# Kernel tuning notes

Measured on AMD Instinct MI355X. Metric: run time of the kernel, lower is better.

The kernel has to match this reference:

```python
import jax, jax.numpy as jnp
import numpy as np

D_MODEL, D_STATE, D_INNER, DT_RANK, K = 64, 16, 128, 4, 4
EPS = 1e-6  # RMSNorm eps


def setup_inputs() -> dict:
    key = jax.random.key(0)
    ks = jax.random.split(key, 12)
    B, L = 8, 4096
    s = 0.02
    x = jax.random.normal(ks[0], (B, L, D_MODEL), dtype=jnp.float32)
    w_norm = jnp.ones((D_MODEL,), jnp.float32)
    W_in = jax.random.normal(ks[1], (2 * D_INNER, D_MODEL), jnp.float32) * s
    b_in = jnp.zeros((2 * D_INNER,), jnp.float32)
    W_conv = jax.random.normal(ks[2], (D_INNER, D_INNER, K), jnp.float32) * s
    b_conv = jnp.zeros((D_INNER,), jnp.float32)
    W_xp = jax.random.normal(ks[3], (DT_RANK + 2 * D_STATE, D_INNER), jnp.float32) * s
    b_xp = jnp.zeros((DT_RANK + 2 * D_STATE,), jnp.float32)
    W_dt = jax.random.normal(ks[4], (D_INNER, DT_RANK), jnp.float32) * s
    b_dt = jnp.zeros((D_INNER,), jnp.float32)
    W_out = jax.random.normal(ks[5], (D_MODEL, D_INNER), jnp.float32) * s
    b_out = jnp.zeros((D_MODEL,), jnp.float32)
    A_log = jnp.log(jnp.tile(jnp.arange(1, D_STATE + 1, dtype=jnp.float32), (D_INNER, 1)))
    D_param = jnp.ones((D_INNER,), jnp.float32)
    return dict(x=x, w_norm=w_norm, W_in=W_in, b_in=b_in, W_conv=W_conv, b_conv=b_conv,
                W_xp=W_xp, b_xp=b_xp, W_dt=W_dt, b_dt=b_dt, W_out=W_out, b_out=b_out,
                A_log=A_log, D_param=D_param)


def _mamba_block(xn, W_in, b_in, W_conv, b_conv, W_xp, b_xp, W_dt, b_dt, W_out, b_out, A_log, D_param):
    B, L, _ = xn.shape
    xz = xn @ W_in.T + b_in                      # (B,L,2*d_inner)
    u, z = jnp.split(xz, 2, axis=-1)
    z = jax.nn.silu(z)
    # conv1d: NCH, causal-style pad (K-1) both sides then truncate to L
    uc = jax.lax.conv_general_dilated(
        u.transpose(0, 2, 1), W_conv, window_strides=(1,), padding=[(K - 1, K - 1)],
        dimension_numbers=("NCH", "OIH", "NCH"))[:, :, :L] + b_conv[None, :, None]
    u = jax.nn.silu(uc.transpose(0, 2, 1))       # (B,L,d_inner)
    xp = u @ W_xp.T + b_xp
    dt, Bm, Cm = jnp.split(xp, [DT_RANK, DT_RANK + D_STATE], axis=-1)
    delta = jax.nn.softplus(dt @ W_dt.T + b_dt)  # (B,L,d_inner)
    A = -jnp.exp(A_log)                          # (d_inner, n)
    A_bar = jnp.exp(jnp.einsum('bld,dn->bldn', delta, A))
    B_bar_x = jnp.einsum('bld,bln,bld->bldn', delta, Bm, u)

    def step(h, inp):
        a, bx, c = inp                           # (B,d,n),(B,d,n),(B,n)
        h = a * h + bx
        y = jnp.einsum('bdn,bn->bd', h, c)
        return h, y

    h0 = jnp.zeros((B, D_INNER, D_STATE), xn.dtype)
    xs = (A_bar.transpose(1, 0, 2, 3), B_bar_x.transpose(1, 0, 2, 3), Cm.transpose(1, 0, 2))
    _, ys = jax.lax.scan(step, h0, xs)           # (L,B,d_inner)
    y = ys.transpose(1, 0, 2) + D_param * u
    y = y * z
    return y @ W_out.T + b_out


def reference(x, w_norm, W_in, b_in, W_conv, b_conv, W_xp, b_xp, W_dt, b_dt, W_out, b_out, A_log, D_param):
    xn = x * jax.lax.rsqrt(jnp.mean(x * x, axis=-1, keepdims=True) + EPS) * w_norm
    return x + _mamba_block(xn, W_in, b_in, W_conv, b_conv, W_xp, b_xp, W_dt, b_dt, W_out, b_out, A_log, D_param)
```

## Files before the change

kernel.cpp:

```cpp
#include <hip/hip_runtime.h>
#include <math.h>

#define D_MODEL 64
#define D_STATE 16
#define D_INNER 128
#define DT_RANK 4
#define BB 8
#define LL 4096
#define NTOK (BB*LL)
#define EPSV 1e-6f
#define NCHUNK 64
#define LC (LL/NCHUNK)
#define PAD 136

typedef __attribute__((ext_vector_type(8))) short bf16x8;
typedef __attribute__((ext_vector_type(4))) float f32x4;

__device__ __forceinline__ float sig_(float v) { return 1.f / (1.f + __expf(-v)); }
__device__ __forceinline__ float softplus_(float v) {
    return (v > 20.f) ? v : __logf(1.f + __expf(v));
}
__device__ __forceinline__ unsigned short f2bf(float x) {
    unsigned int u = __float_as_uint(x);
    u += 0x7fff + ((u >> 16) & 1);
    return (unsigned short)(u >> 16);
}
__device__ __forceinline__ float bf2f(unsigned short u) {
    return __uint_as_float(((unsigned int)u) << 16);
}
__device__ __forceinline__ unsigned int pack2bf(float a, float b) {
    return (unsigned int)f2bf(a) | ((unsigned int)f2bf(b) << 16);
}

__global__ __launch_bounds__(256) void pack_all(
    const float* __restrict__ W_in, const float* __restrict__ w_norm,
    const float* __restrict__ W_conv, const float* __restrict__ W_xp,
    const float* __restrict__ W_out,
    unsigned short* __restrict__ Win_bf, unsigned short* __restrict__ Bp,
    unsigned short* __restrict__ Wxp_bf, unsigned short* __restrict__ Wout_bf)
{
    int i = blockIdx.x * 256 + threadIdx.x;
    if (i < 16384) {
        Win_bf[i] = f2bf(W_in[i] * w_norm[i & 63]);
    } else if (i < 81920) {
        int j = i - 16384;
        int kk = j >> 14, o = (j >> 7) & 127, c = j & 127;
        Bp[j] = f2bf(W_conv[o * 512 + c * 4 + kk]);
    } else if (i < 88064) {
        int j = i - 81920;
        Wxp_bf[j] = ((j >> 7) < 36) ? f2bf(W_xp[j]) : (unsigned short)0;
    } else if (i < 96256) {
        int j = i - 88064;
        Wout_bf[j] = f2bf(W_out[j]);
    }
}

__global__ __launch_bounds__(256) void k1_fused(
    const float* __restrict__ x, const unsigned short* __restrict__ Win_bf,
    const float* __restrict__ b_in,
    unsigned short* __restrict__ u_bf, unsigned short* __restrict__ z_bf)
{
    __shared__ unsigned short axs[64 * 72];
    int tid = threadIdx.x;
    int tb = blockIdx.x * 64;
    {
        int t = tid >> 2, qt = tid & 3;
        float4 v[4];
        float ss = 0.f;
        #pragma unroll
        for (int j = 0; j < 4; ++j) {
            v[j] = *(const float4*)&x[(tb + t) * 64 + qt * 16 + j * 4];
            ss += v[j].x*v[j].x + v[j].y*v[j].y + v[j].z*v[j].z + v[j].w*v[j].w;
        }
        ss += __shfl_xor(ss, 1, 64);
        ss += __shfl_xor(ss, 2, 64);
        float r = rsqrtf(ss * (1.f / 64.f) + EPSV);
        unsigned short tmp[16];
        #pragma unroll
        for (int j = 0; j < 4; ++j) {
            tmp[4*j+0] = f2bf(v[j].x * r); tmp[4*j+1] = f2bf(v[j].y * r);
            tmp[4*j+2] = f2bf(v[j].z * r); tmp[4*j+3] = f2bf(v[j].w * r);
        }
        *(bf16x8*)&axs[t * 72 + qt * 16]     = *(bf16x8*)&tmp[0];
        *(bf16x8*)&axs[t * 72 + qt * 16 + 8] = *(bf16x8*)&tmp[8];
    }
    __syncthreads();
    int wave = tid >> 6, lane = tid & 63;
    int quad = lane >> 4, l16 = lane & 15;
    f32x4 acc[16];
    #pragma unroll
    for (int nt = 0; nt < 16; ++nt) acc[nt] = (f32x4){0.f, 0.f, 0.f, 0.f};
    bf16x8 a0 = *(const bf16x8*)&axs[(wave * 16 + l16) * 72 + quad * 8];
    bf16x8 a1 = *(const bf16x8*)&axs[(wave * 16 + l16) * 72 + 32 + quad * 8];
    #pragma unroll
    for (int nt = 0; nt < 16; ++nt) {
        bf16x8 b0 = *(const bf16x8*)&Win_bf[(nt * 16 + l16) * 64 + quad * 8];
        bf16x8 b1 = *(const bf16x8*)&Win_bf[(nt * 16 + l16) * 64 + 32 + quad * 8];
        acc[nt] = __builtin_amdgcn_mfma_f32_16x16x32_bf16(a0, b0, acc[nt], 0, 0, 0);
        acc[nt] = __builtin_amdgcn_mfma_f32_16x16x32_bf16(a1, b1, acc[nt], 0, 0, 0);
    }
    #pragma unroll
    for (int nt = 0; nt < 16; ++nt) {
        int o = nt * 16 + l16;
        float bo = b_in[o];
        #pragma unroll
        for (int r = 0; r < 4; ++r) {
            int t = tb + wave * 16 + quad * 4 + r;
            float v = acc[nt][r] + bo;
            if (o < 128) u_bf[t * 128 + o] = f2bf(v);
            else         z_bf[t * 128 + (o - 128)] = f2bf(v * sig_(v));
        }
    }
}

__global__ __launch_bounds__(256) void k2k3a_fused(
    const unsigned short* __restrict__ u_bf, const unsigned short* __restrict__ Bp,
    const float* __restrict__ b_conv,
    const unsigned short* __restrict__ Wxp_bf, const float* __restrict__ b_xp,
    const float* __restrict__ W_dt, const float* __restrict__ b_dt,
    const float* __restrict__ A_log,
    unsigned short* __restrict__ u_cbf, unsigned short* __restrict__ delta_bf,
    float* __restrict__ Bm, float* __restrict__ Cm,
    float* __restrict__ P, float* __restrict__ Q)
{
    __shared__ unsigned short uls[64 * PAD];
    __shared__ unsigned short dls[64 * PAD];
    __shared__ float bls[64 * 16];
    __shared__ float dts[64][4];
    __shared__ float Wd[512];
    __shared__ float bds[128];
    int tid = threadIdx.x;
    if (tid < 128) *(float4*)&Wd[tid * 4] = *(const float4*)&W_dt[tid * 4];
    else if (tid < 160) *(float4*)&bds[(tid - 128) * 4] = *(const float4*)&b_dt[(tid - 128) * 4];
    int wave = tid >> 6, lane = tid & 63;
    int quad = lane >> 4, l16 = lane & 15;
    int tb = blockIdx.x * 64;
    int bbase = tb & ~4095;
    int t0 = tb + wave * 16;
    f32x4 acc[8];
    #pragma unroll
    for (int og = 0; og < 8; ++og) acc[og] = (f32x4){0.f, 0.f, 0.f, 0.f};
    int row_base = t0 + l16 - 3;
    #pragma unroll
    for (int kk = 0; kk < 4; ++kk) {
        int row = row_base + kk;
        #pragma unroll
        for (int cs = 0; cs < 4; ++cs) {
            int kbase = cs * 32 + quad * 8;
            bf16x8 a = {0,0,0,0,0,0,0,0};
            if (row >= bbase)
                a = *(const bf16x8*)&u_bf[row * 128 + kbase];
            #pragma unroll
            for (int og = 0; og < 8; ++og) {
                bf16x8 b = *(const bf16x8*)&Bp[kk * 16384 + (og * 16 + l16) * 128 + kbase];
                acc[og] = __builtin_amdgcn_mfma_f32_16x16x32_bf16(a, b, acc[og], 0, 0, 0);
            }
        }
    }
    #pragma unroll
    for (int og = 0; og < 8; ++og) {
        int o = og * 16 + l16;
        float bc = b_conv[o];
        #pragma unroll
        for (int r = 0; r < 4; ++r) {
            int tloc = wave * 16 + quad * 4 + r;
            float v = acc[og][r] + bc;
            unsigned short ub = f2bf(v * sig_(v));
            u_cbf[(tb + tloc) * 128 + o] = ub;
            uls[tloc * PAD + o] = ub;
        }
    }
    __syncthreads();
    f32x4 xacc[3];
    #pragma unroll
    for (int nt = 0; nt < 3; ++nt) xacc[nt] = (f32x4){0.f, 0.f, 0.f, 0.f};
    #pragma unroll
    for (int cs = 0; cs < 4; ++cs) {
        int kbase = cs * 32 + quad * 8;
        bf16x8 a = *(const bf16x8*)&uls[(wave * 16 + l16) * PAD + kbase];
        #pragma unroll
        for (int nt = 0; nt < 3; ++nt) {
            bf16x8 b = *(const bf16x8*)&Wxp_bf[(nt * 16 + l16) * 128 + kbase];
            xacc[nt] = __builtin_amdgcn_mfma_f32_16x16x32_bf16(a, b, xacc[nt], 0, 0, 0);
        }
    }
    #pragma unroll
    for (int nt = 0; nt < 3; ++nt) {
        int j = nt * 16 + l16;
        float bx = (j < 36) ? b_xp[j] : 0.f;
        #pragma unroll
        for (int r = 0; r < 4; ++r) {
            int tloc = wave * 16 + quad * 4 + r;
            int t = tb + tloc;
            float val = xacc[nt][r] + bx;
            if (j < 4) {
                dts[tloc][j] = val;
            } else if (j < 20) {
                Bm[t * 16 + (j - 4)] = val;
                bls[tloc * 16 + (j - 4)] = val;
            } else if (j < 36) {
                Cm[t * 16 + (j - 20)] = val;
            }
        }
    }
    __syncthreads();
    {
        int tokloc = tid >> 2, dgrp = tid & 3;
        float dt0 = dts[tokloc][0], dt1 = dts[tokloc][1],
              dt2 = dts[tokloc][2], dt3 = dts[tokloc][3];
        int g = tb + tokloc;
        #pragma unroll
        for (int d4 = 0; d4 < 8; ++d4) {
            int d = dgrp * 32 + d4 * 4;
            float4 w0 = *(const float4*)&Wd[(d + 0) * 4];
            float4 w1 = *(const float4*)&Wd[(d + 1) * 4];
            float4 w2 = *(const float4*)&Wd[(d + 2) * 4];
            float4 w3 = *(const float4*)&Wd[(d + 3) * 4];
            float4 bdv = *(const float4*)&bds[d];
            float4 r;
            r.x = softplus_(bdv.x + dt0*w0.x + dt1*w0.y + dt2*w0.z + dt3*w0.w);
            r.y = softplus_(bdv.y + dt0*w1.x + dt1*w1.y + dt2*w1.z + dt3*w1.w);
            r.z = softplus_(bdv.z + dt0*w2.x + dt1*w2.y + dt2*w2.z + dt3*w2.w);
            r.w = softplus_(bdv.w + dt0*w3.x + dt1*w3.y + dt2*w3.z + dt3*w3.w);
            uint2 pk; pk.x = pack2bf(r.x, r.y); pk.y = pack2bf(r.z, r.w);
            *(uint2*)&delta_bf[g * 128 + d] = pk;
            *(uint2*)&dls[tokloc * PAD + d] = pk;
        }
    }
    __syncthreads();
    {
        int d = tid >> 1;
        int nb = (tid & 1) * 8;
        float4 Av0 = *(const float4*)&A_log[d * 16 + nb];
        float4 Av1 = *(const float4*)&A_log[d * 16 + nb + 4];
        float A0 = -__expf(Av0.x), A1 = -__expf(Av0.y),
              A2 = -__expf(Av0.z), A3 = -__expf(Av0.w);
        float A4 = -__expf(Av1.x), A5 = -__expf(Av1.y),
              A6 = -__expf(Av1.z), A7 = -__expf(Av1.w);
        float P0=1.f,P1=1.f,P2=1.f,P3=1.f,P4=1.f,P5=1.f,P6=1.f,P7=1.f;
        float Q0=0.f,Q1=0.f,Q2=0.f,Q3=0.f,Q4=0.f,Q5=0.f,Q6=0.f,Q7=0.f;
        for (int t = 0; t < LC; ++t) {
            float dl = bf2f(dls[t * PAD + d]);
            float uu = bf2f(uls[t * PAD + d]);
            float4 bm0 = *(const float4*)&bls[t * 16 + nb];
            float4 bm1 = *(const float4*)&bls[t * 16 + nb + 4];
            float du = dl * uu;
            float a0 = __expf(dl * A0), a1 = __expf(dl * A1),
                  a2 = __expf(dl * A2), a3 = __expf(dl * A3);
            float a4 = __expf(dl * A4), a5 = __expf(dl * A5),
                  a6 = __expf(dl * A6), a7 = __expf(dl * A7);
            P0 *= a0; P1 *= a1; P2 *= a2; P3 *= a3;
            P4 *= a4; P5 *= a5; P6 *= a6; P7 *= a7;
            Q0 = a0 * Q0 + du * bm0.x; Q1 = a1 * Q1 + du * bm0.y;
            Q2 = a2 * Q2 + du * bm0.z; Q3 = a3 * Q3 + du * bm0.w;
            Q4 = a4 * Q4 + du * bm1.x; Q5 = a5 * Q5 + du * bm1.y;
            Q6 = a6 * Q6 + du * bm1.z; Q7 = a7 * Q7 + du * bm1.w;
        }
        int idx = blockIdx.x * 2048 + d * 16 + nb;
        *(float4*)&P[idx]     = (float4){P0, P1, P2, P3};
        *(float4*)&P[idx + 4] = (float4){P4, P5, P6, P7};
        *(float4*)&Q[idx]     = (float4){Q0, Q1, Q2, Q3};
        *(float4*)&Q[idx + 4] = (float4){Q4, Q5, Q6, Q7};
    }
}

__global__ __launch_bounds__(256) void k4b_carry(
    const float* __restrict__ P, const float* __restrict__ Q, float* __restrict__ Hinit)
{
    int tid = blockIdx.x * 256 + threadIdx.x;
    int b = tid >> 11, dn = tid & 2047;
    float carry = 0.f;
    for (int c0 = 0; c0 < NCHUNK; c0 += 8) {
        float p[8], q[8];
        #pragma unroll
        for (int j = 0; j < 8; ++j) {
            int idx = (b * NCHUNK + c0 + j) * 2048 + dn;
            p[j] = P[idx]; q[j] = Q[idx];
        }
        #pragma unroll
        for (int j = 0; j < 8; ++j) {
            int idx = (b * NCHUNK + c0 + j) * 2048 + dn;
            Hinit[idx] = carry;
            carry = p[j] * carry + q[j];
        }
    }
}

__global__ __launch_bounds__(256) void k4c5_fused(
    const unsigned short* __restrict__ delta_bf, const unsigned short* __restrict__ u_cbf,
    const float* __restrict__ Bm, const float* __restrict__ Cm,
    const unsigned short* __restrict__ z_bf, const float* __restrict__ A_log,
    const float* __restrict__ D_param, const float* __restrict__ Hinit,
    const unsigned short* __restrict__ Wout_bf, const float* __restrict__ b_out,
    const float* __restrict__ x, float* __restrict__ out)
{
    __shared__ unsigned short dls[LC * 128];
    __shared__ unsigned short uls[LC * 128];
    __shared__ float bls[LC * 16];
    __shared__ float cls[LC * 16];
    __shared__ unsigned short yzls[LC * PAD];
    int bid = blockIdx.x;
    int tid = threadIdx.x, lane = tid & 63;
    int g0 = bid * 64;
    for (int i = tid; i < LC * 16; i += 256) {
        int row = i >> 4, q = i & 15;
        *(float4*)&dls[row * 128 + q * 8] =
            *(const float4*)&delta_bf[(g0 + row) * 128 + q * 8];
        *(float4*)&uls[row * 128 + q * 8] =
            *(const float4*)&u_cbf[(g0 + row) * 128 + q * 8];
        *(float4*)&yzls[row * PAD + q * 8] =
            *(const float4*)&z_bf[(g0 + row) * 128 + q * 8];
    }
    for (int i = tid; i < LC * 4; i += 256) {
        int row = i >> 2, q = i & 3;
        *(float4*)&bls[row * 16 + q * 4] = *(const float4*)&Bm[(g0 + row) * 16 + q * 4];
        *(float4*)&cls[row * 16 + q * 4] = *(const float4*)&Cm[(g0 + row) * 16 + q * 4];
    }
    int d = tid >> 1;
    int nb = (tid & 1) * 8;
    float4 Av0 = *(const float4*)&A_log[d * 16 + nb];
    float4 Av1 = *(const float4*)&A_log[d * 16 + nb + 4];
    float A0 = -__expf(Av0.x), A1 = -__expf(Av0.y), A2 = -__expf(Av0.z), A3 = -__expf(Av0.w);
    float A4 = -__expf(Av1.x), A5 = -__expf(Av1.y), A6 = -__expf(Av1.z), A7 = -__expf(Av1.w);
    int hbase = bid * 2048 + d * 16 + nb;
    float4 h0 = *(const float4*)&Hinit[hbase];
    float4 h1 = *(const float4*)&Hinit[hbase + 4];
    float Dp = D_param[d];
    __syncthreads();
    for (int t = 0; t < LC; ++t) {
        float dl = bf2f(dls[t * 128 + d]);
        float uu = bf2f(uls[t * 128 + d]);
        float4 bm0 = *(const float4*)&bls[t * 16 + nb];
        float4 bm1 = *(const float4*)&bls[t * 16 + nb + 4];
        float4 cm0 = *(const float4*)&cls[t * 16 + nb];
        float4 cm1 = *(const float4*)&cls[t * 16 + nb + 4];
        float du = dl * uu;
        float a0 = __expf(dl * A0), a1 = __expf(dl * A1),
              a2 = __expf(dl * A2), a3 = __expf(dl * A3);
        float a4 = __expf(dl * A4), a5 = __expf(dl * A5),
              a6 = __expf(dl * A6), a7 = __expf(dl * A7);
        h0.x = a0 * h0.x + du * bm0.x; h0.y = a1 * h0.y + du * bm0.y;
        h0.z = a2 * h0.z + du * bm0.z; h0.w = a3 * h0.w + du * bm0.w;
        h1.x = a4 * h1.x + du * bm1.x; h1.y = a5 * h1.y + du * bm1.y;
        h1.z = a6 * h1.z + du * bm1.z; h1.w = a7 * h1.w + du * bm1.w;
        float yv = h0.x * cm0.x + h0.y * cm0.y + h0.z * cm0.z + h0.w * cm0.w
                 + h1.x * cm1.x + h1.y * cm1.y + h1.z * cm1.z + h1.w * cm1.w;
        yv += __shfl_xor(yv, 1, 64);
        if ((tid & 1) == 0) {
            float y = yv + Dp * uu;
            y *= bf2f(yzls[t * PAD + d]);
            yzls[t * PAD + d] = f2bf(y);
        }
    }
    __syncthreads();
    int wave = tid >> 6;
    int quad = lane >> 4, l16 = lane & 15;
    f32x4 oacc[4];
    #pragma unroll
    for (int nt = 0; nt < 4; ++nt) oacc[nt] = (f32x4){0.f, 0.f, 0.f, 0.f};
    #pragma unroll
    for (int cs = 0; cs < 4; ++cs) {
        int kbase = cs * 32 + quad * 8;
        bf16x8 a = *(const bf16x8*)&yzls[(wave * 16 + l16) * PAD + kbase];
        #pragma unroll
        for (int nt = 0; nt < 4; ++nt) {
            bf16x8 bb = *(const bf16x8*)&Wout_bf[(nt * 16 + l16) * 128 + kbase];
            oacc[nt] = __builtin_amdgcn_mfma_f32_16x16x32_bf16(a, bb, oacc[nt], 0, 0, 0);
        }
    }
    #pragma unroll
    for (int nt = 0; nt < 4; ++nt) {
        int m = nt * 16 + l16;
        float bo = b_out[m];
        #pragma unroll
        for (int r = 0; r < 4; ++r) {
            int t = g0 + wave * 16 + quad * 4 + r;
            out[t * 64 + m] = oacc[nt][r] + bo + x[t * 64 + m];
        }
    }
}

extern "C" void kernel_launch(void* const* d_in, const int* in_sizes, int n_in,
                              void* d_out, int out_size, void* d_ws, size_t ws_size,
                              hipStream_t stream)
{
    const float* x       = (const float*)d_in[0];
    const float* w_norm  = (const float*)d_in[1];
    const float* W_in    = (const float*)d_in[2];
    const float* b_in    = (const float*)d_in[3];
    const float* W_conv  = (const float*)d_in[4];
    const float* b_conv  = (const float*)d_in[5];
    const float* W_xp    = (const float*)d_in[6];
    const float* b_xp    = (const float*)d_in[7];
    const float* W_dt    = (const float*)d_in[8];
    const float* b_dt    = (const float*)d_in[9];
    const float* W_out   = (const float*)d_in[10];
    const float* b_out   = (const float*)d_in[11];
    const float* A_log   = (const float*)d_in[12];
    const float* D_param = (const float*)d_in[13];
    float* ws = (float*)d_ws;

    unsigned short* u_bf = (unsigned short*)ws;
    unsigned short* z_bf = (unsigned short*)(ws + 2097152);
    unsigned short* u_cbf= (unsigned short*)(ws + 4194304);
    unsigned short* delta_bf = (unsigned short*)(ws + 6291456);
    float* Bm     = ws + 10485760;
    float* Cm     = ws + 11010048;
    float* P      = ws + 11534336;
    float* Q      = ws + 12582912;
    float* Hinit  = ws + 13631488;
    unsigned short* Bp      = (unsigned short*)(ws + 14680064);
    unsigned short* Wxp_bf  = (unsigned short*)(ws + 14712832);
    unsigned short* Wout_bf = (unsigned short*)(ws + 14715904);
    unsigned short* Win_bf  = (unsigned short*)(ws + 14720000);
    float* out    = (float*)d_out;

    pack_all<<<376, 256, 0, stream>>>(W_in, w_norm, W_conv, W_xp, W_out,
                                      Win_bf, Bp, Wxp_bf, Wout_bf);
    k1_fused<<<512, 256, 0, stream>>>(x, Win_bf, b_in, u_bf, z_bf);
    k2k3a_fused<<<512, 256, 0, stream>>>(u_bf, Bp, b_conv, Wxp_bf, b_xp,
                                         W_dt, b_dt, A_log,
                                         u_cbf, delta_bf, Bm, Cm, P, Q);
    k4b_carry<<<64, 256, 0, stream>>>(P, Q, Hinit);
    k4c5_fused<<<512, 256, 0, stream>>>(delta_bf, u_cbf, Bm, Cm, z_bf, A_log,
                                        D_param, Hinit, Wout_bf, b_out, x, out);
}
```

Before: 184.0 us.

## Fuse RMSNorm+in_proj into conv/x_proj kernel with halo recompute

New measurement: 175.3 us. 4.7% less time.

```diff
diff --git a/kernel.cpp b/kernel.cpp
--- a/kernel.cpp
+++ b/kernel.cpp
@@ -55,80 +55,28 @@
     }
 }
 
-__global__ __launch_bounds__(256) void k1_fused(
+__global__ __launch_bounds__(256) void k123a_fused(
     const float* __restrict__ x, const unsigned short* __restrict__ Win_bf,
     const float* __restrict__ b_in,
-    unsigned short* __restrict__ u_bf, unsigned short* __restrict__ z_bf)
-{
-    __shared__ unsigned short axs[64 * 72];
-    int tid = threadIdx.x;
-    int tb = blockIdx.x * 64;
-    {
-        int t = tid >> 2, qt = tid & 3;
-        float4 v[4];
-        float ss = 0.f;
-        #pragma unroll
-        for (int j = 0; j < 4; ++j) {
-            v[j] = *(const float4*)&x[(tb + t) * 64 + qt * 16 + j * 4];
-            ss += v[j].x*v[j].x + v[j].y*v[j].y + v[j].z*v[j].z + v[j].w*v[j].w;
-        }
-        ss += __shfl_xor(ss, 1, 64);
-        ss += __shfl_xor(ss, 2, 64);
-        float r = rsqrtf(ss * (1.f / 64.f) + EPSV);
-        unsigned short tmp[16];
-        #pragma unroll
-        for (int j = 0; j < 4; ++j) {
-            tmp[4*j+0] = f2bf(v[j].x * r); tmp[4*j+1] = f2bf(v[j].y * r);
-            tmp[4*j+2] = f2bf(v[j].z * r); tmp[4*j+3] = f2bf(v[j].w * r);
-        }
-        *(bf16x8*)&axs[t * 72 + qt * 16]     = *(bf16x8*)&tmp[0];
-        *(bf16x8*)&axs[t * 72 + qt * 16 + 8] = *(bf16x8*)&tmp[8];
-    }
-    __syncthreads();
-    int wave = tid >> 6, lane = tid & 63;
-    int quad = lane >> 4, l16 = lane & 15;
-    f32x4 acc[16];
-    #pragma unroll
-    for (int nt = 0; nt < 16; ++nt) acc[nt] = (f32x4){0.f, 0.f, 0.f, 0.f};
-    bf16x8 a0 = *(const bf16x8*)&axs[(wave * 16 + l16) * 72 + quad * 8];
-    bf16x8 a1 = *(const bf16x8*)&axs[(wave * 16 + l16) * 72 + 32 + quad * 8];
-    #pragma unroll
-    for (int nt = 0; nt < 16; ++nt) {
-        bf16x8 b0 = *(const bf16x8*)&Win_bf[(nt * 16 + l16) * 64 + quad * 8];
-        bf16x8 b1 = *(const bf16x8*)&Win_bf[(nt * 16 + l16) * 64 + 32 + quad * 8];
-        acc[nt] = __builtin_amdgcn_mfma_f32_16x16x32_bf16(a0, b0, acc[nt], 0, 0, 0);
-        acc[nt] = __builtin_amdgcn_mfma_f32_16x16x32_bf16(a1, b1, acc[nt], 0, 0, 0);
-    }
-    #pragma unroll
-    for (int nt = 0; nt < 16; ++nt) {
-        int o = nt * 16 + l16;
-        float bo = b_in[o];
-        #pragma unroll
-        for (int r = 0; r < 4; ++r) {
-            int t = tb + wave * 16 + quad * 4 + r;
-            float v = acc[nt][r] + bo;
-            if (o < 128) u_bf[t * 128 + o] = f2bf(v);
-            else         z_bf[t * 128 + (o - 128)] = f2bf(v * sig_(v));
-        }
-    }
-}
-
-__global__ __launch_bounds__(256) void k2k3a_fused(
-    const unsigned short* __restrict__ u_bf, const unsigned short* __restrict__ Bp,
-    const float* __restrict__ b_conv,
+    const unsigned short* __restrict__ Bp, const float* __restrict__ b_conv,
     const unsigned short* __restrict__ Wxp_bf, const float* __restrict__ b_xp,
     const float* __restrict__ W_dt, const float* __restrict__ b_dt,
     const float* __restrict__ A_log,
-    unsigned short* __restrict__ u_cbf, unsigned short* __restrict__ delta_bf,
+    unsigned short* __restrict__ z_bf, unsigned short* __restrict__ u_cbf,
+    unsigned short* __restrict__ delta_bf,
     float* __restrict__ Bm, float* __restrict__ Cm,
     float* __restrict__ P, float* __restrict__ Q)
 {
-    __shared__ unsigned short uls[64 * PAD];
-    __shared__ unsigned short dls[64 * PAD];
-    __shared__ float bls[64 * 16];
-    __shared__ float dts[64][4];
-    __shared__ float Wd[512];
-    __shared__ float bds[128];
+    __shared__ unsigned char smem[54832];
+    unsigned short* axs  = (unsigned short*)smem;
+    unsigned short* upre = (unsigned short*)(smem + 11520);
+    unsigned short* dls  = upre;
+    unsigned short* uls  = (unsigned short*)(smem + 29744);
+    float* bls = (float*)(smem + 47152);
+    float (*dts)[4] = (float(*)[4])(smem + 51248);
+    float* Wd  = (float*)(smem + 52272);
+    float* bds = (float*)(smem + 54320);
+
     int tid = threadIdx.x;
     if (tid < 128) *(float4*)&Wd[tid * 4] = *(const float4*)&W_dt[tid * 4];
     else if (tid < 160) *(float4*)&bds[(tid - 128) * 4] = *(const float4*)&b_dt[(tid - 128) * 4];
@@ -136,70 +84,138 @@
     int quad = lane >> 4, l16 = lane & 15;
     int tb = blockIdx.x * 64;
     int bbase = tb & ~4095;
-    int t0 = tb + wave * 16;
-    f32x4 acc[8];
+
     #pragma unroll
-    for (int og = 0; og < 8; ++og) acc[og] = (f32x4){0.f, 0.f, 0.f, 0.f};
-    int row_base = t0 + l16 - 3;
+    for (int p = 0; p < 2; ++p) {
+        int lrow = p * 64 + (tid >> 2);
+        if (lrow < 67) {
+            int qt = tid & 3;
+            int g = tb - 3 + lrow;
+            float4 v[4];
+            float ss = 0.f;
+            if (g >= bbase) {
+                #pragma unroll
+                for (int j = 0; j < 4; ++j) {
+                    v[j] = *(const float4*)&x[g * 64 + qt * 16 + j * 4];
+                    ss += v[j].x*v[j].x + v[j].y*v[j].y + v[j].z*v[j].z + v[j].w*v[j].w;
+                }
+            } else {
+                #pragma unroll
+                for (int j = 0; j < 4; ++j) v[j] = (float4){0.f, 0.f, 0.f, 0.f};
+            }
+            ss += __shfl_xor(ss, 1, 64);
+            ss += __shfl_xor(ss, 2, 64);
+            float r = rsqrtf(ss * (1.f / 64.f) + EPSV);
+            unsigned short tmp[16];
+            #pragma unroll
+            for (int j = 0; j < 4; ++j) {
+                tmp[4*j+0] = f2bf(v[j].x * r); tmp[4*j+1] = f2bf(v[j].y * r);
+                tmp[4*j+2] = f2bf(v[j].z * r); tmp[4*j+3] = f2bf(v[j].w * r);
+            }
+            *(bf16x8*)&axs[lrow * 72 + qt * 16]     = *(bf16x8*)&tmp[0];
+            *(bf16x8*)&axs[lrow * 72 + qt * 16 + 8] = *(bf16x8*)&tmp[8];
+        }
+    }
+    __syncthreads();
     #pragma unroll
-    for (int kk = 0; kk < 4; ++kk) {
-        int row = row_base + kk;
+    for (int mt = 0; mt < 5; ++mt) {
+        bf16x8 a0 = *(const bf16x8*)&axs[(mt * 16 + l16) * 72 + quad * 8];
+        bf16x8 a1 = *(const bf16x8*)&axs[(mt * 16 + l16) * 72 + 32 + quad * 8];
+        f32x4 acc[4];
+        #pragma unroll
+        for (int nk = 0; nk < 4; ++nk) acc[nk] = (f32x4){0.f, 0.f, 0.f, 0.f};
+        #pragma unroll
+        for (int nk = 0; nk < 4; ++nk) {
+            int nt = wave * 4 + nk;
+            bf16x8 b0 = *(const bf16x8*)&Win_bf[(nt * 16 + l16) * 64 + quad * 8];
+            bf16x8 b1 = *(const bf16x8*)&Win_bf[(nt * 16 + l16) * 64 + 32 + quad * 8];
+            acc[nk] = __builtin_amdgcn_mfma_f32_16x16x32_bf16(a0, b0, acc[nk], 0, 0, 0);
+            acc[nk] = __builtin_amdgcn_mfma_f32_16x16x32_bf16(a1, b1, acc[nk], 0, 0, 0);
+        }
+        #pragma unroll
+        for (int nk = 0; nk < 4; ++nk) {
+            int o = (wave * 4 + nk) * 16 + l16;
+            float bo = b_in[o];
+            #pragma unroll
+            for (int r = 0; r < 4; ++r) {
+                int lrow = mt * 16 + quad * 4 + r;
+                if (lrow < 67) {
+                    float v = acc[nk][r] + bo;
+                    if (o < 128) {
+                        upre[lrow * PAD + o] = f2bf(v);
+                    } else if (lrow >= 3) {
+                        float zv = v * sig_(v);
+                        z_bf[(tb + lrow - 3) * 128 + (o - 128)] = f2bf(zv);
+                    }
+                }
+            }
+        }
+    }
+    __syncthreads();
+    {
+        f32x4 acc[8];
+        #pragma unroll
+        for (int og = 0; og < 8; ++og) acc[og] = (f32x4){0.f, 0.f, 0.f, 0.f};
+        #pragma unroll
+        for (int kk = 0; kk < 4; ++kk) {
+            int lr = wave * 16 + l16 + kk;
+            #pragma unroll
+            for (int cs = 0; cs < 4; ++cs) {
+                int kbase = cs * 32 + quad * 8;
+                bf16x8 a = *(const bf16x8*)&upre[lr * PAD + kbase];
+                #pragma unroll
+                for (int og = 0; og < 8; ++og) {
+                    bf16x8 b = *(const bf16x8*)&Bp[kk * 16384 + (og * 16 + l16) * 128 + kbase];
+                    acc[og] = __builtin_amdgcn_mfma_f32_16x16x32_bf16(a, b, acc[og], 0, 0, 0);
+                }
+            }
+        }
+        #pragma unroll
+        for (int og = 0; og < 8; ++og) {
+            int o = og * 16 + l16;
+            float bc = b_conv[o];
+            #pragma unroll
+            for (int r = 0; r < 4; ++r) {
+                int tloc = wave * 16 + quad * 4 + r;
+                float v = acc[og][r] + bc;
+                unsigned short ub = f2bf(v * sig_(v));
+                u_cbf[(tb + tloc) * 128 + o] = ub;
+                uls[tloc * PAD + o] = ub;
+            }
+        }
+    }
+    __syncthreads();
+    {
+        f32x4 xacc[3];
+        #pragma unroll
+        for (int nt = 0; nt < 3; ++nt) xacc[nt] = (f32x4){0.f, 0.f, 0.f, 0.f};
         #pragma unroll
         for (int cs = 0; cs < 4; ++cs) {
             int kbase = cs * 32 + quad * 8;
-            bf16x8 a = {0,0,0,0,0,0,0,0};
-            if (row >= bbase)
-                a = *(const bf16x8*)&u_bf[row * 128 + kbase];
-            #pragma unroll
-            for (int og = 0; og < 8; ++og) {
-                bf16x8 b = *(const bf16x8*)&Bp[kk * 16384 + (og * 16 + l16) * 128 + kbase];
-                acc[og] = __builtin_amdgcn_mfma_f32_16x16x32_bf16(a, b, acc[og], 0, 0, 0);
-            }
-        }
-    }
-    #pragma unroll
-    for (int og = 0; og < 8; ++og) {
-        int o = og * 16 + l16;
-        float bc = b_conv[o];
-        #pragma unroll
-        for (int r = 0; r < 4; ++r) {
-            int tloc = wave * 16 + quad * 4 + r;
-            float v = acc[og][r] + bc;
-            unsigned short ub = f2bf(v * sig_(v));
-            u_cbf[(tb + tloc) * 128 + o] = ub;
-            uls[tloc * PAD + o] = ub;
-        }
-    }
-    __syncthreads();
-    f32x4 xacc[3];
-    #pragma unroll
-    for (int nt = 0; nt < 3; ++nt) xacc[nt] = (f32x4){0.f, 0.f, 0.f, 0.f};
-    #pragma unroll
-    for (int cs = 0; cs < 4; ++cs) {
-        int kbase = cs * 32 + quad * 8;
-        bf16x8 a = *(const bf16x8*)&uls[(wave * 16 + l16) * PAD + kbase];
+            bf16x8 a = *(const bf16x8*)&uls[(wave * 16 + l16) * PAD + kbase];
+            #pragma unroll
+            for (int nt = 0; nt < 3; ++nt) {
+                bf16x8 b = *(const bf16x8*)&Wxp_bf[(nt * 16 + l16) * 128 + kbase];
+                xacc[nt] = __builtin_amdgcn_mfma_f32_16x16x32_bf16(a, b, xacc[nt], 0, 0, 0);
+            }
+        }
         #pragma unroll
         for (int nt = 0; nt < 3; ++nt) {
-            bf16x8 b = *(const bf16x8*)&Wxp_bf[(nt * 16 + l16) * 128 + kbase];
-            xacc[nt] = __builtin_amdgcn_mfma_f32_16x16x32_bf16(a, b, xacc[nt], 0, 0, 0);
-        }
-    }
-    #pragma unroll
-    for (int nt = 0; nt < 3; ++nt) {
-        int j = nt * 16 + l16;
-        float bx = (j < 36) ? b_xp[j] : 0.f;
-        #pragma unroll
-        for (int r = 0; r < 4; ++r) {
-            int tloc = wave * 16 + quad * 4 + r;
-            int t = tb + tloc;
-            float val = xacc[nt][r] + bx;
-            if (j < 4) {
-                dts[tloc][j] = val;
-            } else if (j < 20) {
-                Bm[t * 16 + (j - 4)] = val;
-                bls[tloc * 16 + (j - 4)] = val;
-            } else if (j < 36) {
-                Cm[t * 16 + (j - 20)] = val;
+            int j = nt * 16 + l16;
+            float bx = (j < 36) ? b_xp[j] : 0.f;
+            #pragma unroll
+            for (int r = 0; r < 4; ++r) {
+                int tloc = wave * 16 + quad * 4 + r;
+                int t = tb + tloc;
+                float val = xacc[nt][r] + bx;
+                if (j < 4) {
+                    dts[tloc][j] = val;
+                } else if (j < 20) {
+                    Bm[t * 16 + (j - 4)] = val;
+                    bls[tloc * 16 + (j - 4)] = val;
+                } else if (j < 36) {
+                    Cm[t * 16 + (j - 20)] = val;
+                }
             }
         }
     }
@@ -400,27 +416,25 @@
     const float* D_param = (const float*)d_in[13];
     float* ws = (float*)d_ws;
 
-    unsigned short* u_bf = (unsigned short*)ws;
-    unsigned short* z_bf = (unsigned short*)(ws + 2097152);
-    unsigned short* u_cbf= (unsigned short*)(ws + 4194304);
-    unsigned short* delta_bf = (unsigned short*)(ws + 6291456);
-    float* Bm     = ws + 10485760;
-    float* Cm     = ws + 11010048;
-    float* P      = ws + 11534336;
-    float* Q      = ws + 12582912;
-    float* Hinit  = ws + 13631488;
-    unsigned short* Bp      = (unsigned short*)(ws + 14680064);
-    unsigned short* Wxp_bf  = (unsigned short*)(ws + 14712832);
-    unsigned short* Wout_bf = (unsigned short*)(ws + 14715904);
-    unsigned short* Win_bf  = (unsigned short*)(ws + 14720000);
+    unsigned short* z_bf     = (unsigned short*)ws;
+    unsigned short* u_cbf    = (unsigned short*)(ws + 2097152);
+    unsigned short* delta_bf = (unsigned short*)(ws + 4194304);
+    float* Bm     = ws + 6291456;
+    float* Cm     = ws + 6815744;
+    float* P      = ws + 7340032;
+    float* Q      = ws + 8388608;
+    float* Hinit  = ws + 9437184;
+    unsigned short* Bp      = (unsigned short*)(ws + 10485760);
+    unsigned short* Wxp_bf  = (unsigned short*)(ws + 10518528);
+    unsigned short* Wout_bf = (unsigned short*)(ws + 10521600);
+    unsigned short* Win_bf  = (unsigned short*)(ws + 10525696);
     float* out    = (float*)d_out;
 
     pack_all<<<376, 256, 0, stream>>>(W_in, w_norm, W_conv, W_xp, W_out,
                                       Win_bf, Bp, Wxp_bf, Wout_bf);
-    k1_fused<<<512, 256, 0, stream>>>(x, Win_bf, b_in, u_bf, z_bf);
-    k2k3a_fused<<<512, 256, 0, stream>>>(u_bf, Bp, b_conv, Wxp_bf, b_xp,
-                                         W_dt, b_dt, A_log,
-                                         u_cbf, delta_bf, Bm, Cm, P, Q);
+    k123a_fused<<<512, 256, 0, stream>>>(x, Win_bf, b_in, Bp, b_conv,
+                                         Wxp_bf, b_xp, W_dt, b_dt, A_log,
+                                         z_bf, u_cbf, delta_bf, Bm, Cm, P, Q);
     k4b_carry<<<64, 256, 0, stream>>>(P, Q, Hinit);
     k4c5_fused<<<512, 256, 0, stream>>>(delta_bf, u_cbf, Bm, Cm, z_bf, A_log,
                                         D_param, Hinit, Wout_bf, b_out, x, out);
```
